# Optimization experiments

Measured on AMD Instinct MI355X. Metric: run time of the kernel, lower is better.

## Reference

```python
import jax, jax.numpy as jnp
import numpy as np

B, D, H, W, C = 2, 8, 128, 128, 64
HEADS, DH = 4, 16
EPS = 1e-12  # torch F.normalize eps


def setup_inputs() -> dict:
    key = jax.random.key(0)
    ks = jax.random.split(key, 8)
    rn = lambda k, shp, s: jax.random.normal(k, shp, jnp.float32) * s
    return {
        "x_in": rn(ks[0], (B, D, H, W, C), 1.0),
        "Wq": rn(ks[1], (C, HEADS * DH), 0.05),
        "Wk": rn(ks[2], (C, HEADS * DH), 0.05),
        "Wv": rn(ks[3], (C, HEADS * DH), 0.05),
        "rescale": jnp.ones((HEADS, 1, 1), jnp.float32),
        "Wproj": rn(ks[4], (HEADS * DH, C), 0.05),
        "bproj": jnp.zeros((C,), jnp.float32),
        "Wpos1": rn(ks[5], (C, 1, 3, 3, 3), 0.1),
        "Wpos2": rn(ks[6], (C, 1, 3, 3, 3), 0.1),
    }


def _l2norm(x):
    # torch F.normalize(p=2, dim=-1): x / max(||x||, eps)
    return x / jnp.maximum(jnp.linalg.norm(x, axis=-1, keepdims=True), EPS)


def _dwconv3d(x, w):
    # depthwise Conv3d, kernel 3, stride 1, padding 1, groups = channels
    return jax.lax.conv_general_dilated(
        x, w, (1, 1, 1), 'SAME',
        dimension_numbers=('NCDHW', 'OIDHW', 'NCDHW'),
        feature_group_count=w.shape[0])


def reference(x_in, Wq, Wk, Wv, rescale, Wproj, bproj, Wpos1, Wpos2):
    b, d, h, w, c = x_in.shape
    n = d * h * w
    x = x_in.reshape(b, n, c)
    v_inp = x @ Wv                                   # [b, n, heads*dh]
    # [b, heads, dh, n] layout (attention over channel dim)
    q = jnp.transpose((x @ Wq).reshape(b, n, HEADS, DH), (0, 2, 3, 1))
    k = jnp.transpose((x @ Wk).reshape(b, n, HEADS, DH), (0, 2, 3, 1))
    v = jnp.transpose(v_inp.reshape(b, n, HEADS, DH), (0, 2, 3, 1))
    q = _l2norm(q)
    k = _l2norm(k)
    attn = jnp.einsum('bhdn,bhen->bhde', k, q) * rescale  # [b, heads, dh, dh]
    attn = jax.nn.softmax(attn, axis=-1)
    out = jnp.einsum('bhde,bhen->bhdn', attn, v)          # [b, heads, dh, n]
    out = jnp.transpose(out, (0, 3, 1, 2)).reshape(b, n, HEADS * DH)
    out_c = (out @ Wproj + bproj).reshape(b, d, h, w, c)
    # positional branch: depthwise conv -> GELU -> depthwise conv on v_inp
    vv = jnp.transpose(v_inp.reshape(b, d, h, w, c), (0, 4, 1, 2, 3))  # NCDHW
    p = _dwconv3d(vv, Wpos1)
    p = jax.nn.gelu(p, approximate=False)
    p = _dwconv3d(p, Wpos2)
    out_p = jnp.transpose(p, (0, 2, 3, 4, 1))
    return out_c + out_p
```

## Files before the change

### kernel.cpp

```cpp
#include <hip/hip_runtime.h>
#include <math.h>

#define DD 8
#define HH 128
#define WW2 128
#define NPT 131072
#define NTOT 262144
#define NBK 8

typedef __attribute__((ext_vector_type(8))) short short8;
typedef __attribute__((ext_vector_type(4))) float f32x4;
typedef __attribute__((ext_vector_type(4))) unsigned short u16x4;
typedef __attribute__((ext_vector_type(8))) unsigned short u16x8;
typedef unsigned short u16;

static const size_t OFF_P1  = 0;
static const size_t OFF_P2  = 33554432;
static const size_t OFF_V   = 67108864;
static const size_t OFF_PW  = 100663296;
static const size_t OFF_PM  = 100687872;
static const size_t OFF_FLAG= 100704256;
static const size_t OFF_CW  = 100704768;
#define SP_F    0
#define WQ_F    65536
#define WK_F    69632
#define CW_WPROJ 0
#define CW_WPOS1 4096
#define CW_WPOS2 5824
#define CW_RESC  7552
#define CW_BPROJ 7556
#define CW_ATT   7680

__device__ __forceinline__ float bf2f(u16 u){
  unsigned int x = ((unsigned int)u) << 16;
  return __builtin_bit_cast(float, x);
}
__device__ __forceinline__ u16 f2bf(float f){
  unsigned int x = __builtin_bit_cast(unsigned int, f);
  unsigned int r = (x + 0x7fffu + ((x >> 16) & 1u)) >> 16;
  return (u16)r;
}

__device__ __forceinline__ float fgelu(float o){
  float z  = o * 0.70710678118654752f;
  float az = fabsf(z);
  float t1 = __builtin_amdgcn_rcpf(fmaf(0.3275911f, az, 1.f));
  float poly = t1 * fmaf(t1, fmaf(t1, fmaf(t1, fmaf(t1, 1.061405429f,
               -1.453152027f), 1.421413741f), -0.284496736f), 0.254829592f);
  float ex = __expf(-z * z);
  float er = 1.f - poly * ex;
  er = (z < 0.f) ? -er : er;
  return 0.5f * o * (1.f + er);
}

__global__ __launch_bounds__(256) void k_prep(const void* __restrict__ x,
    const void* __restrict__ Wproj, const void* __restrict__ rescale,
    const void* __restrict__ bproj, const void* __restrict__ Wpos1,
    const void* __restrict__ Wpos2, const void* __restrict__ Wq,
    const void* __restrict__ Wk,
    int* __restrict__ flag, float* __restrict__ cw, float* __restrict__ gpart){
  __shared__ int sflag;
  int t = threadIdx.x, blk = blockIdx.x;
  for (int i = blk * 2048 + t; i < (blk + 1) * 2048; i += 256)
    gpart[i] = 0.f;
  if (blk != 0) return;
  if (t < 64){
    u16 u = ((const u16*)x)[2 * t];
    int e = (u >> 7) & 0xFF;
    int plaus = (u == 0) || (u == 0x8000u) || (e >= 100 && e <= 130);
    unsigned long long m = __ballot(plaus);
    if (t == 0){
      sflag = (__popcll(m) < 48) ? 1 : 0;
      *flag = sflag;
    }
  }
  __syncthreads();
  int isf32 = sflag;
  auto conv = [&](const void* src, float* dst, int n){
    for (int i = t; i < n; i += 256)
      dst[i] = isf32 ? ((const float*)src)[i] : bf2f(((const u16*)src)[i]);
  };
  conv(Wproj, cw + CW_WPROJ, 4096);
  conv(Wpos1, cw + CW_WPOS1, 1728);
  conv(Wpos2, cw + CW_WPOS2, 1728);
  conv(rescale, cw + CW_RESC, 4);
  conv(bproj,   cw + CW_BPROJ, 64);
  conv(Wq, gpart + WQ_F, 4096);
  conv(Wk, gpart + WK_F, 4096);
}

__global__ __launch_bounds__(256) void kpack_w(const void* __restrict__ Wv,
                                               const int* __restrict__ flag,
                                               u16* __restrict__ packW){
  int isf32 = *flag;
  int o = blockIdx.x * 256 + threadIdx.x;
  int f = o >> 9, l = (o >> 3) & 63, j = o & 7;
  int tt = f >> 1, s = f & 1;
  int k = s * 32 + (l >> 4) * 8 + j;
  int n = tt * 16 + (l & 15);
  int idx = k * 64 + n;
  float val = isf32 ? ((const float*)Wv)[idx] : bf2f(((const u16*)Wv)[idx]);
  packW[o] = f2bf(val);
}

__device__ __forceinline__ short8 ld8_adapt(const void* p, size_t idx, int isf32){
  if (!isf32) return *(const short8*)((const u16*)p + idx);
  const float4* f = (const float4*)((const float*)p + idx);
  float4 u = f[0], v2 = f[1];
  short8 r;
  r[0] = (short)f2bf(u.x);  r[1] = (short)f2bf(u.y);
  r[2] = (short)f2bf(u.z);  r[3] = (short)f2bf(u.w);
  r[4] = (short)f2bf(v2.x); r[5] = (short)f2bf(v2.y);
  r[6] = (short)f2bf(v2.z); r[7] = (short)f2bf(v2.w);
  return r;
}

__global__ __launch_bounds__(512) void k_qkv(const void* __restrict__ x,
                                             const int* __restrict__ flag,
                                             const u16* __restrict__ packW,
                                             u16* __restrict__ vT,
                                             float* __restrict__ Sp){
  __shared__ u16 sXT[64][136];
  int isf32 = *flag;
  int wave = threadIdx.x >> 6, lane = threadIdx.x & 63;
  int m = lane & 15, quad = lane >> 4;
  const short8* bw = (const short8*)packW;
  short8 bv[8];
#pragma unroll
  for (int f = 0; f < 8; f++) bv[f] = bw[f * 64 + lane];
  int c1 = wave >> 1, c2p = (wave & 1) * 2;
  f32x4 aS[2];
  aS[0] = (f32x4)(0.f); aS[1] = (f32x4)(0.f);

  int pbase = blockIdx.x * 512;
  int b = pbase >> 17;

  for (int s = 0; s < 4; s++){
    int p0 = pbase + s * 128 + wave * 16;
    size_t rowbase = (size_t)(p0 + m) * 64;
    short8 a0 = ld8_adapt(x, rowbase + quad * 8, isf32);
    short8 a1 = ld8_adapt(x, rowbase + 32 + quad * 8, isf32);
    f32x4 av[4];
#pragma unroll
    for (int t = 0; t < 4; t++) av[t] = (f32x4)(0.f);
#pragma unroll
    for (int t = 0; t < 4; t++){
      av[t] = __builtin_amdgcn_mfma_f32_16x16x32_bf16(a0, bv[t * 2 + 0], av[t], 0, 0, 0);
      av[t] = __builtin_amdgcn_mfma_f32_16x16x32_bf16(a1, bv[t * 2 + 1], av[t], 0, 0, 0);
    }
    int nloc = p0 & (NPT - 1);
#pragma unroll
    for (int t = 0; t < 4; t++){
      u16x4 pk;
#pragma unroll
      for (int r = 0; r < 4; r++) pk[r] = f2bf(av[t][r]);
      *(u16x4*)(vT + ((size_t)(b * 64 + t * 16 + m)) * NPT + nloc + quad * 4) = pk;
    }
    if (s) __syncthreads();
#pragma unroll
    for (int j = 0; j < 8; j++){
      sXT[quad * 8 + j][wave * 16 + m]      = (u16)a0[j];
      sXT[32 + quad * 8 + j][wave * 16 + m] = (u16)a1[j];
    }
    __syncthreads();
#pragma unroll
    for (int ks = 0; ks < 4; ks++){
      short8 fA  = *(const short8*)&sXT[c1 * 16 + m][ks * 32 + quad * 8];
      short8 fB0 = *(const short8*)&sXT[(c2p + 0) * 16 + m][ks * 32 + quad * 8];
      short8 fB1 = *(const short8*)&sXT[(c2p + 1) * 16 + m][ks * 32 + quad * 8];
      aS[0] = __builtin_amdgcn_mfma_f32_16x16x32_bf16(fA, fB0, aS[0], 0, 0, 0);
      aS[1] = __builtin_amdgcn_mfma_f32_16x16x32_bf16(fA, fB1, aS[1], 0, 0, 0);
    }
  }
  int bk = blockIdx.x & (NBK - 1);
  float* Sb = Sp + (size_t)(bk * 2 + b) * 4096;
#pragma unroll
  for (int tt = 0; tt < 2; tt++)
#pragma unroll
    for (int r = 0; r < 4; r++)
      atomicAdd(&Sb[(c1 * 16 + quad * 4 + r) * 64 + (c2p + tt) * 16 + m], aS[tt][r]);
}

__global__ __launch_bounds__(256) void k_attn_h(const float* __restrict__ Sp,
    const float* __restrict__ wqk, const float* __restrict__ cw,
    float* __restrict__ Aout){
  __shared__ float sS[64 * 65];
  __shared__ float sWh[1024];
  __shared__ float sT[1024];
  __shared__ float sG[256];
  __shared__ float sNq[16], sNk[16];
  int blk = blockIdx.x, t = threadIdx.x;
  int b = blk >> 2, h = blk & 3;
  for (int i = t; i < 4096; i += 256){
    float s = 0.f;
#pragma unroll
    for (int bk = 0; bk < NBK; bk++) s += Sp[(size_t)(bk * 2 + b) * 4096 + i];
    sS[(i >> 6) * 65 + (i & 63)] = s;
  }
  for (int i = t; i < 1024; i += 256)
    sWh[i] = wqk[(i >> 4) * 64 + h * 16 + (i & 15)];
  __syncthreads();
  int cc = t & 63, eg = t >> 6;
  {
    float a0 = 0.f, a1 = 0.f, a2 = 0.f, a3 = 0.f;
    for (int c2 = 0; c2 < 64; c2++){
      float sv = sS[cc * 65 + c2];
      a0 = fmaf(sv, sWh[c2 * 16 + eg * 4 + 0], a0);
      a1 = fmaf(sv, sWh[c2 * 16 + eg * 4 + 1], a1);
      a2 = fmaf(sv, sWh[c2 * 16 + eg * 4 + 2], a2);
      a3 = fmaf(sv, sWh[c2 * 16 + eg * 4 + 3], a3);
    }
    sT[cc * 16 + eg * 4 + 0] = a0;
    sT[cc * 16 + eg * 4 + 1] = a1;
    sT[cc * 16 + eg * 4 + 2] = a2;
    sT[cc * 16 + eg * 4 + 3] = a3;
  }
  __syncthreads();
  if (t < 16){
    float a = 0.f;
    for (int c = 0; c < 64; c++) a += sWh[c * 16 + t] * sT[c * 16 + t];
    sNq[t] = a;
  }
  __syncthreads();
  for (int i = t; i < 1024; i += 256)
    sWh[i] = wqk[4096 + (i >> 4) * 64 + h * 16 + (i & 15)];
  __syncthreads();
  {
    int d = t >> 4, e = t & 15;
    float a = 0.f;
    for (int c = 0; c < 64; c++) a += sWh[c * 16 + d] * sT[c * 16 + e];
    sG[d * 16 + e] = a;
  }
  __syncthreads();
  {
    float a0 = 0.f, a1 = 0.f, a2 = 0.f, a3 = 0.f;
    for (int c2 = 0; c2 < 64; c2++){
      float sv = sS[cc * 65 + c2];
      a0 = fmaf(sv, sWh[c2 * 16 + eg * 4 + 0], a0);
      a1 = fmaf(sv, sWh[c2 * 16 + eg * 4 + 1], a1);
      a2 = fmaf(sv, sWh[c2 * 16 + eg * 4 + 2], a2);
      a3 = fmaf(sv, sWh[c2 * 16 + eg * 4 + 3], a3);
    }
    __syncthreads();
    sT[cc * 16 + eg * 4 + 0] = a0;
    sT[cc * 16 + eg * 4 + 1] = a1;
    sT[cc * 16 + eg * 4 + 2] = a2;
    sT[cc * 16 + eg * 4 + 3] = a3;
  }
  __syncthreads();
  if (t < 16){
    float a = 0.f;
    for (int c = 0; c < 64; c++) a += sWh[c * 16 + t] * sT[c * 16 + t];
    sNk[t] = a;
  }
  __syncthreads();
  if (t < 16){
    int d = t;
    float nk = fmaxf(sqrtf(sNk[d]), 1e-12f);
    float rs = cw[CW_RESC + h];
    float lg[16]; float mx = -1e30f;
#pragma unroll
    for (int e = 0; e < 16; e++){
      float nq = fmaxf(sqrtf(sNq[e]), 1e-12f);
      float L = sG[d * 16 + e] / (nk * nq) * rs;
      lg[e] = L; mx = fmaxf(mx, L);
    }
    float sum = 0.f;
#pragma unroll
    for (int e = 0; e < 16; e++){ lg[e] = expf(lg[e] - mx); sum += lg[e]; }
    float inv = 1.f / sum;
#pragma unroll
    for (int e = 0; e < 16; e++)
      Aout[((b * 4 + h) << 8) + d * 16 + e] = lg[e] * inv;
  }
}

__global__ __launch_bounds__(256) void k_packM(const float* __restrict__ Aout,
    const float* __restrict__ cw, u16* __restrict__ packM){
  __shared__ float sA[1024];
  __shared__ float sWp[4096];
  __shared__ float sM[4096];
  int b = blockIdx.x, t = threadIdx.x;
  for (int i = t; i < 1024; i += 256) sA[i] = Aout[b * 1024 + i];
  for (int i = t; i < 4096; i += 256) sWp[i] = cw[CW_WPROJ + i];
  __syncthreads();
  for (int i = t; i < 4096; i += 256){
    int he = i >> 6, c = i & 63;
    int h = he >> 4, e = he & 15;
    float acc = 0.f;
#pragma unroll
    for (int d = 0; d < 16; d++)
      acc += sA[h * 256 + d * 16 + e] * sWp[(h * 16 + d) * 64 + c];
    sM[i] = acc;
  }
  __syncthreads();
  for (int i = t; i < 4096; i += 256){
    int f = i >> 9, l = (i >> 3) & 63, j = i & 7;
    int t4 = f >> 1, s2 = f & 1;
    int k = s2 * 32 + (l >> 4) * 8 + j;
    int n = t4 * 16 + (l & 15);
    packM[b * 4096 + i] = f2bf(sM[k * 64 + n]);
  }
}

template <bool GELU>
__global__ __launch_bounds__(256, 4) void k_dwconv(const u16* __restrict__ src,
    const float* __restrict__ wpos, u16* __restrict__ dst){
  int xi = threadIdx.x & 15, ty = threadIdx.x >> 4;
  int zp = ty >> 2, yq = ty & 3;
  int x0 = xi * 8;
  int c  = blockIdx.x;
  int y0 = blockIdx.y * 8 + yq * 2;
  int b  = blockIdx.z;
  int z0 = zp * 2;
  const float* wg = wpos + c * 27;
  float w27[27];
#pragma unroll
  for (int i = 0; i < 27; i++) w27[i] = wg[i];
  const u16* plane = src + (size_t)(b * 64 + c) * NPT;
  float acc[2][2][8];
#pragma unroll
  for (int dz = 0; dz < 2; dz++)
#pragma unroll
    for (int dy = 0; dy < 2; dy++)
#pragma unroll
      for (int xx = 0; xx < 8; xx++) acc[dz][dy][xx] = 0.f;
#pragma unroll
  for (int izz = 0; izz < 4; izz++){
    int zz = z0 - 1 + izz;
    if (zz < 0 || zz >= DD) continue;
    const u16* pz = plane + zz * 16384;
#pragma unroll
    for (int iyy = 0; iyy < 4; iyy++){
      int yyr = y0 - 1 + iyy;
      int yc = yyr < 0 ? 0 : (yyr > HH - 1 ? HH - 1 : yyr);
      float vmask = (yyr == yc) ? 1.f : 0.f;
      const u16* rp = pz + yc * 128 + x0;
      short8 mid = *(const short8*)rp;
      u16 lft = 0, rgt = 0;
      if (x0 > 0)   lft = rp[-1];
      if (x0 < 120) rgt = rp[8];
      float row[10];
      row[0] = bf2f(lft) * vmask;
#pragma unroll
      for (int e = 0; e < 8; e++) row[1 + e] = bf2f((u16)mid[e]) * vmask;
      row[9] = bf2f(rgt) * vmask;
#pragma unroll
      for (int dzi = 0; dzi < 2; dzi++){
        int kd = izz - dzi;
        if (kd < 0 || kd > 2) continue;
#pragma unroll
        for (int dyi = 0; dyi < 2; dyi++){
          int kh = iyy - dyi;
          if (kh < 0 || kh > 2) continue;
#pragma unroll
          for (int kw = 0; kw < 3; kw++){
            float w = w27[kd * 9 + kh * 3 + kw];
#pragma unroll
            for (int xx = 0; xx < 8; xx++)
              acc[dzi][dyi][xx] = fmaf(row[xx + kw], w, acc[dzi][dyi][xx]);
          }
        }
      }
    }
  }
#pragma unroll
  for (int dzi = 0; dzi < 2; dzi++){
    int zo = z0 + dzi;
#pragma unroll
    for (int dyi = 0; dyi < 2; dyi++){
      int yo = y0 + dyi;
      u16x8 pk;
#pragma unroll
      for (int xx = 0; xx < 8; xx++){
        float o = acc[dzi][dyi][xx];
        if (GELU) o = fgelu(o);
        pk[xx] = f2bf(o);
      }
      *(u16x8*)(dst + (size_t)(b * 64 + c) * NPT + zo * 16384 + yo * 128 + x0) = pk;
    }
  }
}

__global__ __launch_bounds__(256) void k_final(const u16* __restrict__ vT, const u16* __restrict__ packM,
                                               const float* __restrict__ bprojf, const u16* __restrict__ p2T,
                                               float* __restrict__ out){
  int wave = threadIdx.x >> 6, lane = threadIdx.x & 63;
  int m = lane & 15, quad = lane >> 4;
  int p0 = blockIdx.x * 64 + wave * 16;
  int b = p0 >> 17;
  int nloc = p0 & (NPT - 1);
  short8 a0, a1;
#pragma unroll
  for (int j = 0; j < 8; j++){
    a0[j] = (short)vT[(size_t)(b * 64 + quad * 8 + j) * NPT + nloc + m];
    a1[j] = (short)vT[(size_t)(b * 64 + 32 + quad * 8 + j) * NPT + nloc + m];
  }
  const short8* bm = (const short8*)(packM + (size_t)b * 4096);
  f32x4 acc[4];
#pragma unroll
  for (int t = 0; t < 4; t++) acc[t] = (f32x4)(0.f);
#pragma unroll
  for (int t = 0; t < 4; t++){
    short8 b0 = bm[(t * 2 + 0) * 64 + lane];
    short8 b1 = bm[(t * 2 + 1) * 64 + lane];
    acc[t] = __builtin_amdgcn_mfma_f32_16x16x32_bf16(a0, b0, acc[t], 0, 0, 0);
    acc[t] = __builtin_amdgcn_mfma_f32_16x16x32_bf16(a1, b1, acc[t], 0, 0, 0);
  }
#pragma unroll
  for (int t = 0; t < 4; t++){
    int c = t * 16 + m;
    float bias = bprojf[c];
    u16x4 pv = *(const u16x4*)(p2T + (size_t)(b * 64 + c) * NPT + nloc + quad * 4);
#pragma unroll
    for (int r = 0; r < 4; r++){
      size_t p = (size_t)p0 + quad * 4 + r;
      out[p * 64 + c] = acc[t][r] + bias + bf2f(pv[r]);
    }
  }
}

extern "C" void kernel_launch(void* const* d_in, const int* in_sizes, int n_in,
                              void* d_out, int out_size, void* d_ws, size_t ws_size,
                              hipStream_t stream){
  (void)in_sizes; (void)n_in; (void)out_size; (void)ws_size;
  const void* x      = d_in[0];
  const void* Wq     = d_in[1];
  const void* Wk     = d_in[2];
  const void* Wv     = d_in[3];
  const void* rescale= d_in[4];
  const void* Wproj  = d_in[5];
  const void* bproj  = d_in[6];
  const void* Wpos1  = d_in[7];
  const void* Wpos2  = d_in[8];

  char* ws = (char*)d_ws;
  u16* p1T   = (u16*)(ws + OFF_P1);
  u16* p2T   = (u16*)(ws + OFF_P2);
  u16* vT    = (u16*)(ws + OFF_V);
  u16* packW = (u16*)(ws + OFF_PW);
  u16* packM = (u16*)(ws + OFF_PM);
  int* flag  = (int*)(ws + OFF_FLAG);
  float* cw  = (float*)(ws + OFF_CW);
  float* Sp  = (float*)(ws + OFF_P1) + SP_F;
  float* wqk = (float*)(ws + OFF_P1) + WQ_F;
  float* Aout= cw + CW_ATT;
  float* out = (float*)d_out;

  k_prep<<<32, 256, 0, stream>>>(x, Wproj, rescale, bproj, Wpos1, Wpos2, Wq, Wk, flag, cw, Sp);
  kpack_w<<<16, 256, 0, stream>>>(Wv, flag, packW);
  k_qkv<<<NTOT / 512, 512, 0, stream>>>(x, flag, packW, vT, Sp);
  k_attn_h<<<8, 256, 0, stream>>>(Sp, wqk, cw, Aout);
  k_packM<<<2, 256, 0, stream>>>(Aout, cw, packM);
  k_dwconv<true><<<dim3(64, 16, 2), 256, 0, stream>>>(vT, cw + CW_WPOS1, p1T);
  k_dwconv<false><<<dim3(64, 16, 2), 256, 0, stream>>>(p1T, cw + CW_WPOS2, p2T);
  k_final<<<NTOT / 64, 256, 0, stream>>>(vT, packM, cw + CW_BPROJ, p2T, out);
}
```

Baseline: 268.5 us.

## Fold Wv into the output matrix and fuse the small kernels into the dwconv launches

```diff
diff --git a/kernel.cpp b/kernel.cpp
--- a/kernel.cpp
+++ b/kernel.cpp
@@ -21,9 +21,11 @@
 static const size_t OFF_PM  = 100687872;
 static const size_t OFF_FLAG= 100704256;
 static const size_t OFF_CW  = 100704768;
+static const size_t OFF_PART= 134217728;
 #define SP_F    0
 #define WQ_F    65536
 #define WK_F    69632
+#define WV_F    73728
 #define CW_WPROJ 0
 #define CW_WPOS1 4096
 #define CW_WPOS2 5824
@@ -53,54 +55,57 @@
   return 0.5f * o * (1.f + er);
 }
 
+__device__ __forceinline__ int probe_isf32(const void* x, int t){
+  u16 u = ((const u16*)x)[2 * (t & 63)];
+  int e = (u >> 7) & 0xFF;
+  int plaus = (u == 0) || (u == 0x8000u) || (e >= 100 && e <= 130);
+  unsigned long long m = __ballot(plaus);
+  return (__popcll(m) < 48) ? 1 : 0;
+}
+
 __global__ __launch_bounds__(256) void k_prep(const void* __restrict__ x,
     const void* __restrict__ Wproj, const void* __restrict__ rescale,
     const void* __restrict__ bproj, const void* __restrict__ Wpos1,
     const void* __restrict__ Wpos2, const void* __restrict__ Wq,
-    const void* __restrict__ Wk,
-    int* __restrict__ flag, float* __restrict__ cw, float* __restrict__ gpart){
+    const void* __restrict__ Wk, const void* __restrict__ Wv,
+    int* __restrict__ flag, float* __restrict__ cw, float* __restrict__ gpart,
+    u16* __restrict__ packW){
   __shared__ int sflag;
   int t = threadIdx.x, blk = blockIdx.x;
-  for (int i = blk * 2048 + t; i < (blk + 1) * 2048; i += 256)
-    gpart[i] = 0.f;
-  if (blk != 0) return;
   if (t < 64){
-    u16 u = ((const u16*)x)[2 * t];
-    int e = (u >> 7) & 0xFF;
-    int plaus = (u == 0) || (u == 0x8000u) || (e >= 100 && e <= 130);
-    unsigned long long m = __ballot(plaus);
-    if (t == 0){
-      sflag = (__popcll(m) < 48) ? 1 : 0;
-      *flag = sflag;
-    }
+    int f = probe_isf32(x, t);
+    if (t == 0) sflag = f;
   }
   __syncthreads();
   int isf32 = sflag;
-  auto conv = [&](const void* src, float* dst, int n){
-    for (int i = t; i < n; i += 256)
-      dst[i] = isf32 ? ((const float*)src)[i] : bf2f(((const u16*)src)[i]);
-  };
-  conv(Wproj, cw + CW_WPROJ, 4096);
-  conv(Wpos1, cw + CW_WPOS1, 1728);
-  conv(Wpos2, cw + CW_WPOS2, 1728);
-  conv(rescale, cw + CW_RESC, 4);
-  conv(bproj,   cw + CW_BPROJ, 64);
-  conv(Wq, gpart + WQ_F, 4096);
-  conv(Wk, gpart + WK_F, 4096);
-}
-
-__global__ __launch_bounds__(256) void kpack_w(const void* __restrict__ Wv,
-                                               const int* __restrict__ flag,
-                                               u16* __restrict__ packW){
-  int isf32 = *flag;
-  int o = blockIdx.x * 256 + threadIdx.x;
-  int f = o >> 9, l = (o >> 3) & 63, j = o & 7;
-  int tt = f >> 1, s = f & 1;
-  int k = s * 32 + (l >> 4) * 8 + j;
-  int n = tt * 16 + (l & 15);
-  int idx = k * 64 + n;
-  float val = isf32 ? ((const float*)Wv)[idx] : bf2f(((const u16*)Wv)[idx]);
-  packW[o] = f2bf(val);
+  if (blk < 32){
+    for (int i = blk * 2048 + t; i < (blk + 1) * 2048; i += 256)
+      gpart[i] = 0.f;
+    if (blk == 0){
+      if (t == 0) *flag = isf32;
+      auto conv = [&](const void* src, float* dst, int n){
+        for (int i = t; i < n; i += 256)
+          dst[i] = isf32 ? ((const float*)src)[i] : bf2f(((const u16*)src)[i]);
+      };
+      conv(Wproj, cw + CW_WPROJ, 4096);
+      conv(Wpos1, cw + CW_WPOS1, 1728);
+      conv(Wpos2, cw + CW_WPOS2, 1728);
+      conv(rescale, cw + CW_RESC, 4);
+      conv(bproj,   cw + CW_BPROJ, 64);
+      conv(Wq, gpart + WQ_F, 4096);
+      conv(Wk, gpart + WK_F, 4096);
+      conv(Wv, gpart + WV_F, 4096);
+    }
+  } else {
+    int o = (blk - 32) * 256 + t;
+    int f = o >> 9, l = (o >> 3) & 63, j = o & 7;
+    int tt = f >> 1, s = f & 1;
+    int k = s * 32 + (l >> 4) * 8 + j;
+    int n = tt * 16 + (l & 15);
+    int idx = k * 64 + n;
+    float val = isf32 ? ((const float*)Wv)[idx] : bf2f(((const u16*)Wv)[idx]);
+    packW[o] = f2bf(val);
+  }
 }
 
 __device__ __forceinline__ short8 ld8_adapt(const void* p, size_t idx, int isf32){
@@ -181,15 +186,15 @@
       atomicAdd(&Sb[(c1 * 16 + quad * 4 + r) * 64 + (c2p + tt) * 16 + m], aS[tt][r]);
 }
 
-__global__ __launch_bounds__(256) void k_attn_h(const float* __restrict__ Sp,
-    const float* __restrict__ wqk, const float* __restrict__ cw,
-    float* __restrict__ Aout){
-  __shared__ float sS[64 * 65];
-  __shared__ float sWh[1024];
-  __shared__ float sT[1024];
-  __shared__ float sG[256];
-  __shared__ float sNq[16], sNk[16];
-  int blk = blockIdx.x, t = threadIdx.x;
+__device__ void attn_side(int blk, int t, float* smem,
+                          const float* __restrict__ Sp, const float* __restrict__ wqk,
+                          const float* __restrict__ cw, float* __restrict__ Aout){
+  float* sS  = smem;
+  float* sWh = smem + 4160;
+  float* sT  = smem + 5184;
+  float* sG  = smem + 6208;
+  float* sNq = smem + 6464;
+  float* sNk = smem + 6480;
   int b = blk >> 2, h = blk & 3;
   for (int i = t; i < 4096; i += 256){
     float s = 0.f;
@@ -275,22 +280,16 @@
   }
 }
 
-__global__ __launch_bounds__(256) void k_packM(const float* __restrict__ Aout,
-    const float* __restrict__ cw, u16* __restrict__ packM){
-  __shared__ float sA[1024];
-  __shared__ float sWp[4096];
-  __shared__ float sM[4096];
-  int b = blockIdx.x, t = threadIdx.x;
-  for (int i = t; i < 1024; i += 256) sA[i] = Aout[b * 1024 + i];
-  for (int i = t; i < 4096; i += 256) sWp[i] = cw[CW_WPROJ + i];
-  __syncthreads();
+__device__ void fold_side(int b, int t, float* sM,
+                          const float* __restrict__ Aout, const float* __restrict__ Wprojf,
+                          const float* __restrict__ Wvf, u16* __restrict__ packM){
   for (int i = t; i < 4096; i += 256){
     int he = i >> 6, c = i & 63;
     int h = he >> 4, e = he & 15;
     float acc = 0.f;
 #pragma unroll
     for (int d = 0; d < 16; d++)
-      acc += sA[h * 256 + d * 16 + e] * sWp[(h * 16 + d) * 64 + c];
+      acc += Aout[b * 1024 + h * 256 + d * 16 + e] * Wprojf[(h * 16 + d) * 64 + c];
     sM[i] = acc;
   }
   __syncthreads();
@@ -299,13 +298,32 @@
     int t4 = f >> 1, s2 = f & 1;
     int k = s2 * 32 + (l >> 4) * 8 + j;
     int n = t4 * 16 + (l & 15);
-    packM[b * 4096 + i] = f2bf(sM[k * 64 + n]);
+    float acc = 0.f;
+#pragma unroll 8
+    for (int he = 0; he < 64; he++)
+      acc += Wvf[k * 64 + he] * sM[he * 64 + n];
+    packM[b * 4096 + i] = f2bf(acc);
   }
 }
 
 template <bool GELU>
 __global__ __launch_bounds__(256, 4) void k_dwconv(const u16* __restrict__ src,
-    const float* __restrict__ wpos, u16* __restrict__ dst){
+    const float* __restrict__ wpos, u16* __restrict__ dst,
+    const float* __restrict__ Sp, const float* __restrict__ wqk,
+    const float* __restrict__ cw, float* __restrict__ Aout,
+    const float* __restrict__ Wprojf, const float* __restrict__ Wvf,
+    u16* __restrict__ packM){
+  constexpr int SMSZ = GELU ? 6496 : 4096;
+  __shared__ float smem[SMSZ];
+  if (blockIdx.x == 64){
+    int side = blockIdx.z * 16 + blockIdx.y;
+    if (GELU){
+      if (side < 8) attn_side(side, threadIdx.x, smem, Sp, wqk, cw, Aout);
+    } else {
+      if (side < 2) fold_side(side, threadIdx.x, smem, Aout, Wprojf, Wvf, packM);
+    }
+    return;
+  }
   int xi = threadIdx.x & 15, ty = threadIdx.x >> 4;
   int zp = ty >> 2, yq = ty & 3;
   int x0 = xi * 8;
@@ -382,20 +400,21 @@
   }
 }
 
-__global__ __launch_bounds__(256) void k_final(const u16* __restrict__ vT, const u16* __restrict__ packM,
-                                               const float* __restrict__ bprojf, const u16* __restrict__ p2T,
+__global__ __launch_bounds__(256) void k_final(const void* __restrict__ x,
+                                               const int* __restrict__ flag,
+                                               const u16* __restrict__ packM,
+                                               const float* __restrict__ bprojf,
+                                               const u16* __restrict__ p2T,
                                                float* __restrict__ out){
+  int isf32 = *flag;
   int wave = threadIdx.x >> 6, lane = threadIdx.x & 63;
   int m = lane & 15, quad = lane >> 4;
   int p0 = blockIdx.x * 64 + wave * 16;
   int b = p0 >> 17;
   int nloc = p0 & (NPT - 1);
-  short8 a0, a1;
-#pragma unroll
-  for (int j = 0; j < 8; j++){
-    a0[j] = (short)vT[(size_t)(b * 64 + quad * 8 + j) * NPT + nloc + m];
-    a1[j] = (short)vT[(size_t)(b * 64 + 32 + quad * 8 + j) * NPT + nloc + m];
-  }
+  size_t rowbase = (size_t)(p0 + m) * 64;
+  short8 a0 = ld8_adapt(x, rowbase + quad * 8, isf32);
+  short8 a1 = ld8_adapt(x, rowbase + 32 + quad * 8, isf32);
   const short8* bm = (const short8*)(packM + (size_t)b * 4096);
   f32x4 acc[4];
 #pragma unroll
@@ -442,17 +461,19 @@
   u16* packM = (u16*)(ws + OFF_PM);
   int* flag  = (int*)(ws + OFF_FLAG);
   float* cw  = (float*)(ws + OFF_CW);
-  float* Sp  = (float*)(ws + OFF_P1) + SP_F;
-  float* wqk = (float*)(ws + OFF_P1) + WQ_F;
+  float* part= (float*)(ws + OFF_PART);
+  float* Sp  = part + SP_F;
+  float* wqk = part + WQ_F;
+  float* Wvf = part + WV_F;
   float* Aout= cw + CW_ATT;
   float* out = (float*)d_out;
 
-  k_prep<<<32, 256, 0, stream>>>(x, Wproj, rescale, bproj, Wpos1, Wpos2, Wq, Wk, flag, cw, Sp);
-  kpack_w<<<16, 256, 0, stream>>>(Wv, flag, packW);
+  k_prep<<<48, 256, 0, stream>>>(x, Wproj, rescale, bproj, Wpos1, Wpos2, Wq, Wk, Wv,
+                                 flag, cw, Sp, packW);
   k_qkv<<<NTOT / 512, 512, 0, stream>>>(x, flag, packW, vT, Sp);
-  k_attn_h<<<8, 256, 0, stream>>>(Sp, wqk, cw, Aout);
-  k_packM<<<2, 256, 0, stream>>>(Aout, cw, packM);
-  k_dwconv<true><<<dim3(64, 16, 2), 256, 0, stream>>>(vT, cw + CW_WPOS1, p1T);
-  k_dwconv<false><<<dim3(64, 16, 2), 256, 0, stream>>>(p1T, cw + CW_WPOS2, p2T);
-  k_final<<<NTOT / 64, 256, 0, stream>>>(vT, packM, cw + CW_BPROJ, p2T, out);
-}
+  k_dwconv<true><<<dim3(65, 16, 2), 256, 0, stream>>>(vT, cw + CW_WPOS1, p1T,
+      Sp, wqk, cw, Aout, cw + CW_WPROJ, Wvf, packM);
+  k_dwconv<false><<<dim3(65, 16, 2), 256, 0, stream>>>(p1T, cw + CW_WPOS2, p2T,
+      Sp, wqk, cw, Aout, cw + CW_WPROJ, Wvf, packM);
+  k_final<<<NTOT / 64, 256, 0, stream>>>(x, flag, packM, cw + CW_BPROJ, p2T, out);
+}
```

Result: slower. 275.7 us (+2.7%).
